# Optimization experiments

Hardware: AMD Instinct MI355X
Metric: run time of the kernel (lower is better)

Reference implementation:

```python
import jax, jax.numpy as jnp
import numpy as np

H = 8   # num_heads
K = 2   # num_timescales (hard-coded in module)


def _apply_rope(x, cos, sin):
    # x: [B,T,H,D]; cos/sin: [1,T,1,D/2]; interleaved even/odd pairs
    xp = x.reshape(*x.shape[:-1], -1, 2)
    xr, xi = xp[..., 0], xp[..., 1]
    rr = xr * cos - xi * sin
    ri = xr * sin + xi * cos
    return jnp.stack([rr, ri], axis=-1).reshape(x.shape)


def setup_inputs() -> dict:
    key = jax.random.key(0)
    ks = jax.random.split(key, 11)
    B, T, C = 4, 2048, 1024
    HK = H * K
    s = 0.02  # xavier-ish scale
    return {
        'x': jax.random.normal(ks[0], (B, T, C), jnp.float32),
        'mask': jnp.ones((B, T), jnp.int32),
        'Wq': jax.random.normal(ks[1], (C, C), jnp.float32) * s,
        'Wk': jax.random.normal(ks[2], (C, C), jnp.float32) * s,
        'Wv': jax.random.normal(ks[3], (C, C), jnp.float32) * s,
        'Wb': jax.random.normal(ks[4], (C, HK), jnp.float32) * s,
        'bb': jax.random.normal(ks[5], (HK,), jnp.float32) * 0.5 + 2.0,
        'Wm': jax.random.normal(ks[6], (C, HK), jnp.float32) * s,
        'bm': jax.random.normal(ks[7], (HK,), jnp.float32) * 0.1,
        'Wo': jax.random.normal(ks[8], (C, C), jnp.float32) * s,
        'bo': jnp.zeros((C,), jnp.float32),
    }


def reference(x, mask, Wq, Wk, Wv, Wb, bb, Wm, bm, Wo, bo):
    B, T, C = x.shape
    D = C // H
    q = (x @ Wq).reshape(B, T, H, D)
    k = (x @ Wk).reshape(B, T, H, D)
    v = (x @ Wv).reshape(B, T, H, D)

    # RoPE cache
    inv_freq = 1.0 / (10000.0 ** (jnp.arange(0, D, 2, dtype=jnp.float32) / D))
    freqs = jnp.arange(T, dtype=jnp.float32)[:, None] * inv_freq[None, :]  # [T,D/2]
    cos = jnp.cos(freqs)[None, :, None, :].astype(x.dtype)
    sin = jnp.sin(freqs)[None, :, None, :].astype(x.dtype)
    q = _apply_rope(q, cos, sin)
    k = _apply_rope(k, cos, sin)

    beta = jax.nn.sigmoid((x @ Wb + bb).reshape(B, T, H, K))  # [B,T,H,K]
    mix = jax.nn.softmax((x @ Wm + bm).reshape(B, T, H, K), axis=-1)

    def step(S, ins):
        # S: [B,H,K,D,D]
        q_t, k_t, v_t, b_t, m_t, mk = ins  # [B,H,D],[B,H,D],[B,H,D],[B,H,K],[B,H,K],[B]
        outer = jnp.einsum('bhd,bhe->bhde', k_t, v_t)          # [B,H,D,D]
        S_new = b_t[..., None, None] * S + outer[:, :, None]   # [B,H,K,D,D]
        S = jnp.where(mk[:, None, None, None, None] > 0, S_new, S)
        y_k = jnp.einsum('bhd,bhkde->bhke', q_t, S)            # [B,H,K,D]
        y_t = jnp.sum(y_k * m_t[..., None], axis=2)            # [B,H,D]
        y_t = jnp.where(mk[:, None, None] > 0, y_t, jnp.zeros_like(y_t))
        return S, y_t

    S0 = jnp.zeros((B, H, K, D, D), x.dtype)
    xs = (jnp.swapaxes(q, 0, 1), jnp.swapaxes(k, 0, 1), jnp.swapaxes(v, 0, 1),
          jnp.swapaxes(beta, 0, 1), jnp.swapaxes(mix, 0, 1), mask.T)
    _, ys = jax.lax.scan(step, S0, xs)           # ys: [T,B,H,D]
    y = jnp.swapaxes(ys, 0, 1).reshape(B, T, C)
    return y @ Wo + bo
```

## Files before the change

kernel.cpp:

```cpp
#include <hip/hip_runtime.h>

typedef __attribute__((ext_vector_type(4))) float f32x4;
typedef __attribute__((ext_vector_type(8))) __bf16 bf16x8;

#define T_DIM 2048
#define B_DIM 4
#define C_DIM 1024
#define H_N 8
#define D_H 128
#define M_ROWS 8192
#define MC ((size_t)M_ROWS * C_DIM)
#define LCH 64
#define NCH (T_DIM / LCH)
#define CHSZ (128 * 128)
#define SWE(r) ((((r) ^ ((r) >> 3)) & 7) << 3)

#define GLDS16(g, l) __builtin_amdgcn_global_load_lds( \
    (const __attribute__((address_space(1))) void*)(g), \
    (__attribute__((address_space(3))) void*)(l), 16, 0, 0)

__global__ void small_prep_k(float2* __restrict__ tab,
                             const float* __restrict__ Wb,
                             const float* __restrict__ Wm,
                             __bf16* __restrict__ WbmT) {
    int bid = blockIdx.x;
    if (bid < 512) {
        int idx = bid * 256 + threadIdx.x;
        int t = idx >> 6, i = idx & 63;
        float freq = expf(-(2.0f * (float)i / 128.0f) * 9.210340371976184f);
        float a = (float)t * freq;
        tab[idx] = make_float2(cosf(a), sinf(a));
    } else {
        int n = bid - 512;
        int col = n & 15;
        const float* W = (n < 16) ? Wb : Wm;
        for (int k = threadIdx.x; k < C_DIM; k += 256)
            WbmT[(size_t)n * C_DIM + k] = (__bf16)W[(size_t)k * 16 + col];
    }
}

__global__ __launch_bounds__(256) void cvt_x_k(const float* __restrict__ in,
                                               __bf16* __restrict__ out) {
    int i = blockIdx.x * 256 + threadIdx.x;
    f32x4 a = ((const f32x4*)in)[i * 2];
    f32x4 b = ((const f32x4*)in)[i * 2 + 1];
    bf16x8 o;
    o[0] = (__bf16)a.x; o[1] = (__bf16)a.y; o[2] = (__bf16)a.z; o[3] = (__bf16)a.w;
    o[4] = (__bf16)b.x; o[5] = (__bf16)b.y; o[6] = (__bf16)b.z; o[7] = (__bf16)b.w;
    ((bf16x8*)out)[i] = o;
}

__global__ __launch_bounds__(256) void wtrans_k(
    const float* __restrict__ W0, const float* __restrict__ W1,
    const float* __restrict__ W2, const float* __restrict__ W3,
    __bf16* __restrict__ out) {
    const float* W = blockIdx.z == 0 ? W0 : blockIdx.z == 1 ? W1 :
                     blockIdx.z == 2 ? W2 : W3;
    __bf16* o = out + (size_t)blockIdx.z * C_DIM * C_DIM;
    __shared__ float t[64][65];
    int tid = threadIdx.x;
    int r0 = blockIdx.y * 64, c0 = blockIdx.x * 64;
    #pragma unroll
    for (int it = 0; it < 4; ++it) {
        int idx = it * 256 + tid;
        int r = idx >> 4, c4 = (idx & 15) * 4;
        f32x4 v = *(const f32x4*)(W + (size_t)(r0 + r) * C_DIM + c0 + c4);
        t[r][c4] = v.x; t[r][c4 + 1] = v.y; t[r][c4 + 2] = v.z; t[r][c4 + 3] = v.w;
    }
    __syncthreads();
    #pragma unroll
    for (int it = 0; it < 2; ++it) {
        int idx = it * 256 + tid;
        int n = idx >> 3, k8 = (idx & 7) * 8;
        bf16x8 ov;
        #pragma unroll
        for (int j = 0; j < 8; ++j) ov[j] = (__bf16)t[k8 + j][n];
        *(bf16x8*)(o + (size_t)(c0 + n) * C_DIM + r0 + k8) = ov;
    }
}

__global__ __launch_bounds__(256) void betamix_mfma(
    const __bf16* __restrict__ xb, const __bf16* __restrict__ WbmT,
    const float* __restrict__ bb, const float* __restrict__ bm,
    float* __restrict__ beta, float* __restrict__ mix) {
    __shared__ __bf16 As[2][32 * 64];

    int tid = threadIdx.x;
    int w = tid >> 6, lane = tid & 63;
    int lr = lane & 15, lg = lane >> 4;
    int ifr = w >> 1, j = w & 1;
    int rows0 = blockIdx.x * 32;

    int srow = tid >> 3;
    int sg = (tid & 7) ^ (srow & 7);
    size_t aoff = (size_t)(rows0 + srow) * C_DIM + sg * 8;
    int ldso = w * 64 * 16;

    f32x4 acc = {};
    const __bf16* Wrow = WbmT + (size_t)(j * 16 + lr) * C_DIM;

    GLDS16(xb + aoff, (char*)As[0] + ldso);
    asm volatile("s_waitcnt vmcnt(0)" ::: "memory");
    __syncthreads();

    for (int t = 0; t < 16; ++t) {
        int cur = t & 1;
        if (t < 15) GLDS16(xb + aoff + (t + 1) * 64, (char*)As[cur ^ 1] + ldso);
        #pragma unroll
        for (int ss = 0; ss < 2; ++ss) {
            int ar = ifr * 16 + lr;
            bf16x8 af = *(const bf16x8*)((char*)As[cur] + ar * 128 + (((ss * 4 + lg) ^ (ar & 7)) << 4));
            bf16x8 bf = *(const bf16x8*)(Wrow + t * 64 + ss * 32 + lg * 8);
            acc = __builtin_amdgcn_mfma_f32_16x16x32_bf16(af, bf, acc, 0, 0, 0);
        }
        asm volatile("s_waitcnt vmcnt(0)" ::: "memory");
        __syncthreads();
    }

    float bias = (j ? bm : bb)[lr];
    #pragma unroll
    for (int r = 0; r < 4; ++r) {
        int row = rows0 + ifr * 16 + lg * 4 + r;
        float v = acc[r] + bias;
        if (j == 0) {
            beta[(size_t)row * 16 + lr] = 1.f / (1.f + expf(-v));
        } else {
            float other = __shfl_xor(v, 1);
            float mx = fmaxf(v, other);
            float e = expf(v - mx), eo = expf(other - mx);
            mix[(size_t)row * 16 + lr] = e / (e + eo);
        }
    }
}

__global__ __launch_bounds__(256) void decay_k(
    const float* __restrict__ beta, const float* __restrict__ mixp,
    const int* __restrict__ mask,
    float* __restrict__ wvm, float* __restrict__ rcm,
    float* __restrict__ qsc, float* __restrict__ cumLg) {
    int gw = blockIdx.x * 4 + (threadIdx.x >> 6);
    int s = threadIdx.x & 63;
    int scan = gw >> 5, c = gw & 31;
    int b = scan >> 4, hh = scan & 15;
    size_t row = (size_t)b * T_DIM + c * LCH + s;
    int mk = mask[row];
    float mf = mk ? 1.f : 0.f;
    float bt = mk ? beta[row * 16 + hh] : 1.f;
    float mx = mk ? mixp[row * 16 + hh] : 0.f;
    float cum = bt;
    #pragma unroll
    for (int off = 1; off < 64; off <<= 1) {
        float p = __shfl(cum, (s >= off) ? s - off : 0);
        if (s >= off) cum *= p;
    }
    float cl = __shfl(cum, 63);
    size_t o = (size_t)scan * T_DIM + c * LCH + s;
    wvm[o] = mf * cl / cum;
    rcm[o] = mf / cum;
    qsc[o] = mf * mx * cum;
    if (s == 63) cumLg[scan * NCH + c] = cl;
}

__global__ __launch_bounds__(256) void gemm_qkv(
    const __bf16* __restrict__ A, const __bf16* __restrict__ BT,
    __bf16* __restrict__ outq, const float2* __restrict__ rope_tab) {
    __shared__ __bf16 As[128 * 64];
    __shared__ __bf16 Bs[128 * 64];
    const int K = C_DIM;

    int tid = threadIdx.x;
    int xcd = blockIdx.x & 7, lid = blockIdx.x >> 3;
    int g = lid >> 6, u = lid & 63;
    int bm = xcd * 8 + (u >> 3), bn = g * 8 + (u & 7);
    int m_base = bm << 7, n_base = bn << 7;
    int w = tid >> 6, lane = tid & 63;
    int lr = lane & 15, lg = lane >> 4;
    int wm = (w >> 1) * 64, wn = (w & 1) * 64;

    size_t aoff[4], boff[4];
    int ldso[4];
    #pragma unroll
    for (int it = 0; it < 4; ++it) {
        int gi = it * 256 + tid;
        int row = gi >> 3;
        int gr = (gi & 7) ^ (row & 7);
        aoff[it] = (size_t)(m_base + row) * K + gr * 8;
        boff[it] = (size_t)(n_base + row) * K + gr * 8;
        ldso[it] = (it * 256 + w * 64) * 16;
    }

    f32x4 acc[4][4] = {};

    for (int k0 = 0; k0 < K; k0 += 64) {
        __syncthreads();
        #pragma unroll
        for (int it = 0; it < 4; ++it) {
            GLDS16(A + aoff[it] + k0, (char*)As + ldso[it]);
            GLDS16(BT + boff[it] + k0, (char*)Bs + ldso[it]);
        }
        __syncthreads();
        #pragma unroll
        for (int ss = 0; ss < 2; ++ss) {
            bf16x8 af[4], bfr[4];
            #pragma unroll
            for (int i = 0; i < 4; ++i) {
                int ar = wm + i * 16 + lr;
                af[i] = *(const bf16x8*)((char*)As + ar * 128 + (((ss * 4 + lg) ^ (ar & 7)) << 4));
                int br = wn + i * 16 + lr;
                bfr[i] = *(const bf16x8*)((char*)Bs + br * 128 + (((ss * 4 + lg) ^ (br & 7)) << 4));
            }
            #pragma unroll
            for (int i = 0; i < 4; ++i)
                #pragma unroll
                for (int j = 0; j < 4; ++j)
                    acc[i][j] = __builtin_amdgcn_mfma_f32_16x16x32_bf16(af[i], bfr[j], acc[i][j], 0, 0, 0);
        }
    }

    #pragma unroll
    for (int i = 0; i < 4; ++i) {
        #pragma unroll
        for (int j = 0; j < 4; ++j) {
            #pragma unroll
            for (int r = 0; r < 4; ++r) {
                int grow = m_base + wm + i * 16 + (lg << 2) + r;
                int gcol = n_base + wn + j * 16 + lr;
                float val = acc[i][j][r];
                int buf = gcol >> 10;
                int col = gcol & 1023;
                if (buf < 2) {
                    float partner = __shfl_xor(val, 1);
                    int t = grow & (T_DIM - 1);
                    int ii = (col & 127) >> 1;
                    float2 cs = rope_tab[t * 64 + ii];
                    val = (col & 1) ? (partner * cs.y + val * cs.x)
                                    : (val * cs.x - partner * cs.y);
                }
                outq[(size_t)buf * MC + (size_t)grow * C_DIM + col] = (__bf16)val;
            }
        }
    }
}

__global__ __launch_bounds__(256) void gemm_bt(
    const __bf16* __restrict__ A, const __bf16* __restrict__ BT,
    float* __restrict__ Cp, int M, int N, int K,
    const float* __restrict__ bias) {
    __shared__ __bf16 As[2][128 * 64];
    __shared__ __bf16 Bs[2][128 * 64];

    int tid = threadIdx.x;
    int nTN = N >> 7;
    int cpx = gridDim.x >> 3;
    int bid = ((int)blockIdx.x & 7) * cpx + ((int)blockIdx.x >> 3);
    int bm = bid / nTN, bn = bid % nTN;
    int m_base = bm << 7, n_base = bn << 7;
    int w = tid >> 6, lane = tid & 63;
    int lr = lane & 15, lg = lane >> 4;
    int wm = (w >> 1) * 64, wn = (w & 1) * 64;

    size_t aoff[4], boff[4];
    int ldso[4];
    #pragma unroll
    for (int it = 0; it < 4; ++it) {
        int gi = it * 256 + tid;
        int row = gi >> 3;
        int g = (gi & 7) ^ (row & 7);
        aoff[it] = (size_t)(m_base + row) * K + g * 8;
        boff[it] = (size_t)(n_base + row) * K + g * 8;
        ldso[it] = (it * 256 + w * 64) * 16;
    }

#define STAGE_G(bufi, k0)                                                   \
    _Pragma("unroll")                                                       \
    for (int it = 0; it < 4; ++it) {                                        \
        GLDS16(A + aoff[it] + (k0), (char*)As[bufi] + ldso[it]);            \
        GLDS16(BT + boff[it] + (k0), (char*)Bs[bufi] + ldso[it]);           \
    }

    f32x4 acc[4][4] = {};

    STAGE_G(0, 0);
    asm volatile("s_waitcnt vmcnt(0)" ::: "memory");
    __syncthreads();

    int nt = K >> 6;
    for (int t = 0; t < nt; ++t) {
        int cur = t & 1;
        if (t + 1 < nt) STAGE_G(cur ^ 1, (t + 1) * 64);
        #pragma unroll
        for (int ss = 0; ss < 2; ++ss) {
            bf16x8 af[4], bfr[4];
            #pragma unroll
            for (int i = 0; i < 4; ++i) {
                int ar = wm + i * 16 + lr;
                af[i] = *(const bf16x8*)((char*)As[cur] + ar * 128 + (((ss * 4 + lg) ^ (ar & 7)) << 4));
                int br = wn + i * 16 + lr;
                bfr[i] = *(const bf16x8*)((char*)Bs[cur] + br * 128 + (((ss * 4 + lg) ^ (br & 7)) << 4));
            }
            #pragma unroll
            for (int i = 0; i < 4; ++i)
                #pragma unroll
                for (int j = 0; j < 4; ++j)
                    acc[i][j] = __builtin_amdgcn_mfma_f32_16x16x32_bf16(af[i], bfr[j], acc[i][j], 0, 0, 0);
        }
        asm volatile("s_waitcnt vmcnt(0)" ::: "memory");
        __syncthreads();
    }
#undef STAGE_G

    #pragma unroll
    for (int i = 0; i < 4; ++i) {
        #pragma unroll
        for (int j = 0; j < 4; ++j) {
            #pragma unroll
            for (int r = 0; r < 4; ++r) {
                int grow = m_base + wm + i * 16 + (lg << 2) + r;
                int gcol = n_base + wn + j * 16 + lr;
                float val = acc[i][j][r] + bias[gcol];
                Cp[(size_t)grow * N + gcol] = val;
            }
        }
    }
}

__global__ __launch_bounds__(256) void chunk_sum_k(
    const __bf16* __restrict__ kg, const __bf16* __restrict__ vg,
    const float* __restrict__ wvm, __bf16* __restrict__ BT) {
    __shared__ __bf16 KT[128 * 64];
    __shared__ __bf16 VT[128 * 64];

    int tid = threadIdx.x;
    int c = blockIdx.x, kk = blockIdx.y, bh = blockIdx.z;
    int b = bh >> 3, h = bh & 7;
    int scan = bh * 2 + kk;
    size_t rowb = (size_t)b * T_DIM + c * LCH;
    size_t wb = (size_t)scan * T_DIM + c * LCH;

    #pragma unroll
    for (int it = 0; it < 4; ++it) {
        int f = tid + it * 256;
        int s = f >> 4, c8 = (f & 15) * 8;
        size_t g = (rowb + s) * C_DIM + h * D_H + c8;
        bf16x8 kv = *(const bf16x8*)(kg + g);
        bf16x8 vv = *(const bf16x8*)(vg + g);
        float ws_ = wvm[wb + s];
        #pragma unroll
        for (int j = 0; j < 8; ++j) {
            int d = c8 + j;
            KT[d * 64 + (s ^ SWE(d))] = (__bf16)(ws_ * (float)kv[j]);
            VT[d * 64 + (s ^ SWE(d))] = vv[j];
        }
    }
    __syncthreads();

    int w = tid >> 6, l = tid & 63;
    int lr = l & 15, lg = l >> 4;
    f32x4 acc[2][8] = {};
    #pragma unroll
    for (int kt = 0; kt < 2; ++kt) {
        int col = kt * 32 + lg * 8;
        bf16x8 aV[2], bK[8];
        #pragma unroll
        for (int et = 0; et < 2; ++et) {
            int e = w * 32 + et * 16 + lr;
            aV[et] = *(const bf16x8*)&VT[e * 64 + (col ^ SWE(e))];
        }
        #pragma unroll
        for (int dt = 0; dt < 8; ++dt) {
            int d = dt * 16 + lr;
            bK[dt] = *(const bf16x8*)&KT[d * 64 + (col ^ SWE(d))];
        }
        #pragma unroll
        for (int et = 0; et < 2; ++et)
            #pragma unroll
            for (int dt = 0; dt < 8; ++dt)
                acc[et][dt] = __builtin_amdgcn_mfma_f32_16x16x32_bf16(aV[et], bK[dt], acc[et][dt], 0, 0, 0);
    }

    __bf16* bout = BT + ((size_t)scan * NCH + c) * CHSZ;
    #pragma unroll
    for (int et = 0; et < 2; ++et)
        #pragma unroll
        for (int dt = 0; dt < 8; ++dt)
            #pragma unroll
            for (int r = 0; r < 4; ++r) {
                int e = w * 32 + et * 16 + lg * 4 + r;
                bout[e * 128 + dt * 16 + lr] = (__bf16)acc[et][dt][r];
            }
}

__global__ __launch_bounds__(256) void chunk_scan_k(
    __bf16* __restrict__ BT, const float* __restrict__ cumLg) {
    int bid = blockIdx.x;
    int scan = bid >> 3, part = bid & 7;
    int tid = threadIdx.x;
    int e = part * 16 + (tid >> 4);
    int d0 = (tid & 15) * 8;
    __bf16* base = BT + (size_t)scan * NCH * CHSZ + e * 128 + d0;
    const float* cl = cumLg + scan * NCH;
    float acc[8] = {};
    for (int c = 0; c < NCH; ++c) {
        bf16x8 bv = *(const bf16x8*)(base + (size_t)c * CHSZ);
        float g = cl[c];
        bf16x8 so;
        #pragma unroll
        for (int j = 0; j < 8; ++j) so[j] = (__bf16)acc[j];
        *(bf16x8*)(base + (size_t)c * CHSZ) = so;
        #pragma unroll
        for (int j = 0; j < 8; ++j) acc[j] = g * acc[j] + (float)bv[j];
    }
}

__global__ __launch_bounds__(256, 3) void chunk_out_k(
    const __bf16* __restrict__ qg, const __bf16* __restrict__ kg,
    const __bf16* __restrict__ vg, const __bf16* __restrict__ ST,
    const float* __restrict__ rcm, const float* __restrict__ qscg,
    __bf16* __restrict__ yg) {
    __shared__ __bf16 STs[2][64 * 128];
    __shared__ __bf16 VT[64 * 64];
    __shared__ __bf16 Ps[64 * 72];
    __shared__ float rcumf[2][64], qscf[2][64];

    int tid = threadIdx.x;
    int c = blockIdx.x, eh = blockIdx.y, bh = blockIdx.z;
    int b = bh >> 3, h = bh & 7;
    int e0 = eh * 64;
    size_t rowb = (size_t)b * T_DIM + c * LCH;
    int w = tid >> 6, l = tid & 63;
    int lr = l & 15, lg = l >> 4;

    {
        const __bf16* stb = ST + ((size_t)(bh * 2) * NCH + c) * CHSZ + (size_t)e0 * 128;
        int r = tid >> 4, gran = tid & 15;
        size_t goff = (size_t)r * 128 + ((gran ^ (r & 7)) * 8);
        #pragma unroll
        for (int kk = 0; kk < 2; ++kk) {
            const __bf16* sp = stb + (size_t)kk * NCH * CHSZ;
            #pragma unroll
            for (int it = 0; it < 4; ++it) {
                GLDS16(sp + goff + (size_t)it * 16 * 128,
                       (char*)STs[kk] + (it * 256 + w * 64) * 16);
            }
        }
    }

    if (tid < 128) {
        int s = tid & 63, kk = tid >> 6;
        size_t o = (size_t)(bh * 2 + kk) * T_DIM + c * LCH + s;
        rcumf[kk][s] = rcm[o];
        qscf[kk][s] = qscg[o];
    }

    bf16x8 vreg[2];
    #pragma unroll
    for (int it = 0; it < 2; ++it) {
        int f = tid + it * 256;
        int s = f >> 3, c8 = (f & 7) * 8;
        vreg[it] = *(const bf16x8*)(vg + (rowb + s) * C_DIM + h * D_H + e0 + c8);
    }

    const __bf16* qrow = qg + (rowb + w * 16 + lr) * C_DIM + h * D_H;
    bf16x8 aQ[4];
    #pragma unroll
    for (int kt = 0; kt < 4; ++kt)
        aQ[kt] = *(const bf16x8*)(qrow + kt * 32 + lg * 8);

    const __bf16* kbase = kg + rowb * C_DIM + h * D_H;
    bf16x8 bkreg[16];
    #pragma unroll
    for (int st = 0; st < 4; ++st)
        #pragma unroll
        for (int kt = 0; kt < 4; ++kt)
            bkreg[st * 4 + kt] = *(const bf16x8*)(kbase + (size_t)(st * 16 + lr) * C_DIM + kt * 32 + lg * 8);

    #pragma unroll
    for (int it = 0; it < 2; ++it) {
        int f = tid + it * 256;
        int s = f >> 3, c8 = (f & 7) * 8;
        #pragma unroll
        for (int j = 0; j < 8; ++j) {
            int el = c8 + j;
            VT[el * 64 + (s ^ SWE(el))] = vreg[it][j];
        }
    }

    f32x4 Praw[4];
    #pragma unroll
    for (int st = 0; st < 4; ++st) {
        f32x4 p = {};
        #pragma unroll
        for (int kt = 0; kt < 4; ++kt)
            p = __builtin_amdgcn_mfma_f32_16x16x32_bf16(aQ[kt], bkreg[st * 4 + kt], p, 0, 0, 0);
        Praw[st] = p;
    }

    asm volatile("s_waitcnt vmcnt(0)" ::: "memory");
    __syncthreads();

    f32x4 yA[4] = {};
    #pragma unroll
    for (int kk = 0; kk < 2; ++kk) {
        #pragma unroll
        for (int st = 0; st < 4; ++st) {
            #pragma unroll
            for (int r = 0; r < 4; ++r) {
                int tl = w * 16 + lg * 4 + r;
                int sc = st * 16 + lr;
                float pv = (sc <= tl) ? Praw[st][r] * rcumf[kk][sc] * qscf[kk][tl] : 0.f;
                Ps[tl * 72 + sc] = (__bf16)pv;
            }
        }
        bf16x8 aP[2];
        #pragma unroll
        for (int k2 = 0; k2 < 2; ++k2)
            aP[k2] = *(const bf16x8*)&Ps[(w * 16 + lr) * 72 + k2 * 32 + lg * 8];

        __builtin_amdgcn_s_setprio(1);
        #pragma unroll
        for (int et = 0; et < 4; ++et) {
            int el = et * 16 + lr;
            f32x4 ys = {};
            #pragma unroll
            for (int kt = 0; kt < 4; ++kt) {
                bf16x8 bs = *(const bf16x8*)((char*)STs[kk] + el * 256 + (((kt * 4 + lg) ^ (el & 7)) << 4));
                ys = __builtin_amdgcn_mfma_f32_16x16x32_bf16(aQ[kt], bs, ys, 0, 0, 0);
            }
            f32x4 yp = {};
            #pragma unroll
            for (int k2 = 0; k2 < 2; ++k2) {
                bf16x8 bv = *(const bf16x8*)&VT[el * 64 + ((k2 * 32 + lg * 8) ^ SWE(el))];
                yp = __builtin_amdgcn_mfma_f32_16x16x32_bf16(aP[k2], bv, yp, 0, 0, 0);
            }
            #pragma unroll
            for (int r = 0; r < 4; ++r)
                yA[et][r] += ys[r] * qscf[kk][w * 16 + lg * 4 + r] + yp[r];
        }
        __builtin_amdgcn_s_setprio(0);
    }
    #pragma unroll
    for (int et = 0; et < 4; ++et)
        #pragma unroll
        for (int r = 0; r < 4; ++r) {
            size_t row = rowb + w * 16 + lg * 4 + r;
            yg[row * C_DIM + h * D_H + e0 + et * 16 + lr] = (__bf16)yA[et][r];
        }
}

extern "C" void kernel_launch(void* const* d_in, const int* in_sizes, int n_in,
                              void* d_out, int out_size, void* d_ws, size_t ws_size,
                              hipStream_t stream) {
    const float* x    = (const float*)d_in[0];
    const int*   mask = (const int*)d_in[1];
    const float* Wq   = (const float*)d_in[2];
    const float* Wk   = (const float*)d_in[3];
    const float* Wv   = (const float*)d_in[4];
    const float* Wb   = (const float*)d_in[5];
    const float* bb   = (const float*)d_in[6];
    const float* Wm   = (const float*)d_in[7];
    const float* bm   = (const float*)d_in[8];
    const float* Wo   = (const float*)d_in[9];
    const float* bo   = (const float*)d_in[10];
    float* out = (float*)d_out;

    __bf16* q    = (__bf16*)d_ws;
    __bf16* k    = q + MC;
    __bf16* v    = k + MC;
    __bf16* xb   = v + MC;
    __bf16* WT   = xb + MC;
    __bf16* BT   = WT + (size_t)4 * C_DIM * C_DIM;
    float* beta  = (float*)(BT + (size_t)64 * NCH * CHSZ);
    float* mixb  = beta + M_ROWS * 16;
    float* cumL  = mixb + M_ROWS * 16;
    float* wvm   = cumL + 64 * NCH;
    float* rcm   = wvm + (size_t)64 * T_DIM;
    float* qscg  = rcm + (size_t)64 * T_DIM;
    float2* rope = (float2*)(qscg + (size_t)64 * T_DIM);
    __bf16* WbmT = (__bf16*)(rope + T_DIM * 64);
    __bf16* ysum = xb;

    small_prep_k<<<dim3(544), dim3(256), 0, stream>>>(rope, Wb, Wm, WbmT);
    cvt_x_k<<<dim3(MC / 8 / 256), dim3(256), 0, stream>>>(x, xb);
    wtrans_k<<<dim3(16, 16, 4), dim3(256), 0, stream>>>(Wq, Wk, Wv, Wo, WT);
    betamix_mfma<<<dim3(M_ROWS / 32), dim3(256), 0, stream>>>(xb, WbmT, bb, bm, beta, mixb);
    decay_k<<<dim3(512), dim3(256), 0, stream>>>(beta, mixb, mask, wvm, rcm, qscg, cumL);

    const size_t CC = (size_t)C_DIM * C_DIM;
    gemm_qkv<<<dim3(1536), dim3(256), 0, stream>>>(xb, WT, q, rope);

    chunk_sum_k<<<dim3(NCH, 2, 32), dim3(256), 0, stream>>>(k, v, wvm, BT);
    chunk_scan_k<<<dim3(512), dim3(256), 0, stream>>>(BT, cumL);
    chunk_out_k<<<dim3(NCH, 2, 32), dim3(256), 0, stream>>>(q, k, v, BT, rcm, qscg, ysum);

    gemm_bt<<<dim3((M_ROWS / 128) * (C_DIM / 128)), dim3(256), 0, stream>>>(
        ysum, WT + 3 * CC, out, M_ROWS, C_DIM, C_DIM, bo);
}
```

Measured before the change: 220.8 us.

## Merge prep kernels into one launch and double-buffer the QKV GEMM

The three small preprocessing kernels (x bf16 conversion, weight transposes, RoPE table and Wb/Wm transpose) become a single launch that branches on block index, removing two launch gaps. The QKV GEMM moves to a 3D grid with one z-slice per projection and double-buffered LDS staging, so the next K tile loads while MFMAs run on the current one. The block-to-tile mapping also changes to an XCD-interleaved scheme like gemm_bt. LDS use doubles to 64KB per block, which may lower occupancy, and the merged prep kernel allocates shared memory even for blocks that do not use it.

```diff
diff --git a/kernel.cpp b/kernel.cpp
--- a/kernel.cpp
+++ b/kernel.cpp
@@ -19,63 +19,63 @@
     (const __attribute__((address_space(1))) void*)(g), \
     (__attribute__((address_space(3))) void*)(l), 16, 0, 0)
 
-__global__ void small_prep_k(float2* __restrict__ tab,
-                             const float* __restrict__ Wb,
-                             const float* __restrict__ Wm,
-                             __bf16* __restrict__ WbmT) {
-    int bid = blockIdx.x;
-    if (bid < 512) {
-        int idx = bid * 256 + threadIdx.x;
-        int t = idx >> 6, i = idx & 63;
-        float freq = expf(-(2.0f * (float)i / 128.0f) * 9.210340371976184f);
-        float a = (float)t * freq;
-        tab[idx] = make_float2(cosf(a), sinf(a));
-    } else {
-        int n = bid - 512;
-        int col = n & 15;
-        const float* W = (n < 16) ? Wb : Wm;
-        for (int k = threadIdx.x; k < C_DIM; k += 256)
-            WbmT[(size_t)n * C_DIM + k] = (__bf16)W[(size_t)k * 16 + col];
-    }
-}
-
-__global__ __launch_bounds__(256) void cvt_x_k(const float* __restrict__ in,
-                                               __bf16* __restrict__ out) {
-    int i = blockIdx.x * 256 + threadIdx.x;
-    f32x4 a = ((const f32x4*)in)[i * 2];
-    f32x4 b = ((const f32x4*)in)[i * 2 + 1];
-    bf16x8 o;
-    o[0] = (__bf16)a.x; o[1] = (__bf16)a.y; o[2] = (__bf16)a.z; o[3] = (__bf16)a.w;
-    o[4] = (__bf16)b.x; o[5] = (__bf16)b.y; o[6] = (__bf16)b.z; o[7] = (__bf16)b.w;
-    ((bf16x8*)out)[i] = o;
-}
-
-__global__ __launch_bounds__(256) void wtrans_k(
+__global__ __launch_bounds__(256) void prep_all_k(
+    const float* __restrict__ x, __bf16* __restrict__ xb,
     const float* __restrict__ W0, const float* __restrict__ W1,
     const float* __restrict__ W2, const float* __restrict__ W3,
-    __bf16* __restrict__ out) {
-    const float* W = blockIdx.z == 0 ? W0 : blockIdx.z == 1 ? W1 :
-                     blockIdx.z == 2 ? W2 : W3;
-    __bf16* o = out + (size_t)blockIdx.z * C_DIM * C_DIM;
+    __bf16* __restrict__ WT,
+    float2* __restrict__ tab,
+    const float* __restrict__ Wb, const float* __restrict__ Wm,
+    __bf16* __restrict__ WbmT) {
     __shared__ float t[64][65];
+    int bid = blockIdx.x;
     int tid = threadIdx.x;
-    int r0 = blockIdx.y * 64, c0 = blockIdx.x * 64;
-    #pragma unroll
-    for (int it = 0; it < 4; ++it) {
-        int idx = it * 256 + tid;
-        int r = idx >> 4, c4 = (idx & 15) * 4;
-        f32x4 v = *(const f32x4*)(W + (size_t)(r0 + r) * C_DIM + c0 + c4);
-        t[r][c4] = v.x; t[r][c4 + 1] = v.y; t[r][c4 + 2] = v.z; t[r][c4 + 3] = v.w;
-    }
-    __syncthreads();
-    #pragma unroll
-    for (int it = 0; it < 2; ++it) {
-        int idx = it * 256 + tid;
-        int n = idx >> 3, k8 = (idx & 7) * 8;
-        bf16x8 ov;
-        #pragma unroll
-        for (int j = 0; j < 8; ++j) ov[j] = (__bf16)t[k8 + j][n];
-        *(bf16x8*)(o + (size_t)(c0 + n) * C_DIM + r0 + k8) = ov;
+    if (bid < 4096) {
+        int i = bid * 256 + tid;
+        f32x4 a = ((const f32x4*)x)[i * 2];
+        f32x4 b = ((const f32x4*)x)[i * 2 + 1];
+        bf16x8 o;
+        o[0] = (__bf16)a.x; o[1] = (__bf16)a.y; o[2] = (__bf16)a.z; o[3] = (__bf16)a.w;
+        o[4] = (__bf16)b.x; o[5] = (__bf16)b.y; o[6] = (__bf16)b.z; o[7] = (__bf16)b.w;
+        ((bf16x8*)xb)[i] = o;
+    } else if (bid < 5120) {
+        int tt = bid - 4096;
+        int wz = tt >> 8, rem = tt & 255;
+        int r0 = (rem >> 4) * 64, c0 = (rem & 15) * 64;
+        const float* W = wz == 0 ? W0 : wz == 1 ? W1 : wz == 2 ? W2 : W3;
+        __bf16* o = WT + (size_t)wz * C_DIM * C_DIM;
+        #pragma unroll
+        for (int it = 0; it < 4; ++it) {
+            int idx = it * 256 + tid;
+            int r = idx >> 4, c4 = (idx & 15) * 4;
+            f32x4 v = *(const f32x4*)(W + (size_t)(r0 + r) * C_DIM + c0 + c4);
+            t[r][c4] = v.x; t[r][c4 + 1] = v.y; t[r][c4 + 2] = v.z; t[r][c4 + 3] = v.w;
+        }
+        __syncthreads();
+        #pragma unroll
+        for (int it = 0; it < 2; ++it) {
+            int idx = it * 256 + tid;
+            int n = idx >> 3, k8 = (idx & 7) * 8;
+            bf16x8 ov;
+            #pragma unroll
+            for (int j = 0; j < 8; ++j) ov[j] = (__bf16)t[k8 + j][n];
+            *(bf16x8*)(o + (size_t)(c0 + n) * C_DIM + r0 + k8) = ov;
+        }
+    } else {
+        int sp = bid - 5120;
+        if (sp < 512) {
+            int idx = sp * 256 + tid;
+            int tq = idx >> 6, i = idx & 63;
+            float freq = expf(-(2.0f * (float)i / 128.0f) * 9.210340371976184f);
+            float a = (float)tq * freq;
+            tab[idx] = make_float2(cosf(a), sinf(a));
+        } else {
+            int n = sp - 512;
+            int col = n & 15;
+            const float* W = (n < 16) ? Wb : Wm;
+            for (int k = tid; k < C_DIM; k += 256)
+                WbmT[(size_t)n * C_DIM + k] = (__bf16)W[(size_t)k * 16 + col];
+        }
     }
 }
 
@@ -161,17 +161,22 @@
     if (s == 63) cumLg[scan * NCH + c] = cl;
 }
 
-__global__ __launch_bounds__(256) void gemm_qkv(
-    const __bf16* __restrict__ A, const __bf16* __restrict__ BT,
-    __bf16* __restrict__ outq, const float2* __restrict__ rope_tab) {
-    __shared__ __bf16 As[128 * 64];
-    __shared__ __bf16 Bs[128 * 64];
-    const int K = C_DIM;
+__global__ __launch_bounds__(256) void gemm_qkv3(
+    const __bf16* __restrict__ A, const __bf16* __restrict__ WT,
+    __bf16* __restrict__ outbase, const float2* __restrict__ rope_tab) {
+    __shared__ __bf16 As[2][128 * 64];
+    __shared__ __bf16 Bs[2][128 * 64];
+    const int K = C_DIM, N = C_DIM;
 
     int tid = threadIdx.x;
-    int xcd = blockIdx.x & 7, lid = blockIdx.x >> 3;
-    int g = lid >> 6, u = lid & 63;
-    int bm = xcd * 8 + (u >> 3), bn = g * 8 + (u & 7);
+    int z = blockIdx.z;
+    const __bf16* BT = WT + (size_t)z * C_DIM * C_DIM;
+    __bf16* Cp = outbase + (size_t)z * MC;
+    bool do_rope = z < 2;
+
+    int nTN = N >> 7;
+    int bid = ((int)blockIdx.x & 7) * 64 + ((int)blockIdx.x >> 3);
+    int bm = bid / nTN, bn = bid % nTN;
     int m_base = bm << 7, n_base = bn << 7;
     int w = tid >> 6, lane = tid & 63;
     int lr = lane & 15, lg = lane >> 4;
@@ -183,31 +188,38 @@
     for (int it = 0; it < 4; ++it) {
         int gi = it * 256 + tid;
         int row = gi >> 3;
-        int gr = (gi & 7) ^ (row & 7);
-        aoff[it] = (size_t)(m_base + row) * K + gr * 8;
-        boff[it] = (size_t)(n_base + row) * K + gr * 8;
+        int g = (gi & 7) ^ (row & 7);
+        aoff[it] = (size_t)(m_base + row) * K + g * 8;
+        boff[it] = (size_t)(n_base + row) * K + g * 8;
         ldso[it] = (it * 256 + w * 64) * 16;
     }
 
+#define STAGE_G(bufi, k0)                                                   \
+    _Pragma("unroll")                                                       \
+    for (int it = 0; it < 4; ++it) {                                        \
+        GLDS16(A + aoff[it] + (k0), (char*)As[bufi] + ldso[it]);            \
+        GLDS16(BT + boff[it] + (k0), (char*)Bs[bufi] + ldso[it]);           \
+    }
+
     f32x4 acc[4][4] = {};
 
-    for (int k0 = 0; k0 < K; k0 += 64) {
-        __syncthreads();
-        #pragma unroll
-        for (int it = 0; it < 4; ++it) {
-            GLDS16(A + aoff[it] + k0, (char*)As + ldso[it]);
-            GLDS16(BT + boff[it] + k0, (char*)Bs + ldso[it]);
-        }
-        __syncthreads();
+    STAGE_G(0, 0);
+    asm volatile("s_waitcnt vmcnt(0)" ::: "memory");
+    __syncthreads();
+
+    const int nt = K >> 6;
+    for (int t = 0; t < nt; ++t) {
+        int cur = t & 1;
+        if (t + 1 < nt) STAGE_G(cur ^ 1, (t + 1) * 64);
         #pragma unroll
         for (int ss = 0; ss < 2; ++ss) {
             bf16x8 af[4], bfr[4];
             #pragma unroll
             for (int i = 0; i < 4; ++i) {
                 int ar = wm + i * 16 + lr;
-                af[i] = *(const bf16x8*)((char*)As + ar * 128 + (((ss * 4 + lg) ^ (ar & 7)) << 4));
+                af[i] = *(const bf16x8*)((char*)As[cur] + ar * 128 + (((ss * 4 + lg) ^ (ar & 7)) << 4));
                 int br = wn + i * 16 + lr;
-                bfr[i] = *(const bf16x8*)((char*)Bs + br * 128 + (((ss * 4 + lg) ^ (br & 7)) << 4));
+                bfr[i] = *(const bf16x8*)((char*)Bs[cur] + br * 128 + (((ss * 4 + lg) ^ (br & 7)) << 4));
             }
             #pragma unroll
             for (int i = 0; i < 4; ++i)
@@ -215,7 +227,10 @@
                 for (int j = 0; j < 4; ++j)
                     acc[i][j] = __builtin_amdgcn_mfma_f32_16x16x32_bf16(af[i], bfr[j], acc[i][j], 0, 0, 0);
         }
-    }
+        asm volatile("s_waitcnt vmcnt(0)" ::: "memory");
+        __syncthreads();
+    }
+#undef STAGE_G
 
     #pragma unroll
     for (int i = 0; i < 4; ++i) {
@@ -226,17 +241,15 @@
                 int grow = m_base + wm + i * 16 + (lg << 2) + r;
                 int gcol = n_base + wn + j * 16 + lr;
                 float val = acc[i][j][r];
-                int buf = gcol >> 10;
-                int col = gcol & 1023;
-                if (buf < 2) {
+                if (do_rope) {
                     float partner = __shfl_xor(val, 1);
                     int t = grow & (T_DIM - 1);
-                    int ii = (col & 127) >> 1;
+                    int ii = (gcol & 127) >> 1;
                     float2 cs = rope_tab[t * 64 + ii];
-                    val = (col & 1) ? (partner * cs.y + val * cs.x)
-                                    : (val * cs.x - partner * cs.y);
+                    val = (gcol & 1) ? (partner * cs.y + val * cs.x)
+                                     : (val * cs.x - partner * cs.y);
                 }
-                outq[(size_t)buf * MC + (size_t)grow * C_DIM + col] = (__bf16)val;
+                Cp[(size_t)grow * C_DIM + gcol] = (__bf16)val;
             }
         }
     }
@@ -317,8 +330,7 @@
             for (int r = 0; r < 4; ++r) {
                 int grow = m_base + wm + i * 16 + (lg << 2) + r;
                 int gcol = n_base + wn + j * 16 + lr;
-                float val = acc[i][j][r] + bias[gcol];
-                Cp[(size_t)grow * N + gcol] = val;
+                Cp[(size_t)grow * N + gcol] = acc[i][j][r] + bias[gcol];
             }
         }
     }
@@ -579,14 +591,13 @@
     __bf16* WbmT = (__bf16*)(rope + T_DIM * 64);
     __bf16* ysum = xb;
 
-    small_prep_k<<<dim3(544), dim3(256), 0, stream>>>(rope, Wb, Wm, WbmT);
-    cvt_x_k<<<dim3(MC / 8 / 256), dim3(256), 0, stream>>>(x, xb);
-    wtrans_k<<<dim3(16, 16, 4), dim3(256), 0, stream>>>(Wq, Wk, Wv, Wo, WT);
+    prep_all_k<<<dim3(5664), dim3(256), 0, stream>>>(
+        x, xb, Wq, Wk, Wv, Wo, WT, rope, Wb, Wm, WbmT);
     betamix_mfma<<<dim3(M_ROWS / 32), dim3(256), 0, stream>>>(xb, WbmT, bb, bm, beta, mixb);
     decay_k<<<dim3(512), dim3(256), 0, stream>>>(beta, mixb, mask, wvm, rcm, qscg, cumL);
 
     const size_t CC = (size_t)C_DIM * C_DIM;
-    gemm_qkv<<<dim3(1536), dim3(256), 0, stream>>>(xb, WT, q, rope);
+    gemm_qkv3<<<dim3(512, 1, 3), dim3(256), 0, stream>>>(xb, WT, q, rope);
 
     chunk_sum_k<<<dim3(NCH, 2, 32), dim3(256), 0, stream>>>(k, v, wvm, BT);
     chunk_scan_k<<<dim3(512), dim3(256), 0, stream>>>(BT, cumL);
```

New measurement: 218.1 us. No clear change (-1.2%).

## Merge prep kernels into one launch and retile output GEMM to 64x128

Applied to the files above, without the earlier changes.

Three preprocessing kernels (x conversion, weight transposes, RoPE table and beta/mix weight packing) are folded into a single launch that dispatches on block index, cutting launch overhead and gaps between kernels. The output projection GEMM moves from 128x128 tiles with double-buffered LDS to 64x128 tiles with single buffering. This doubles the block count to 1024 for better CU occupancy and balance on an 8192x1024 output. In exchange, the GEMM loses global-load/compute overlap and re-reads B twice as often.

```diff
diff --git a/kernel.cpp b/kernel.cpp
--- a/kernel.cpp
+++ b/kernel.cpp
@@ -19,63 +19,63 @@
     (const __attribute__((address_space(1))) void*)(g), \
     (__attribute__((address_space(3))) void*)(l), 16, 0, 0)
 
-__global__ void small_prep_k(float2* __restrict__ tab,
-                             const float* __restrict__ Wb,
-                             const float* __restrict__ Wm,
-                             __bf16* __restrict__ WbmT) {
-    int bid = blockIdx.x;
-    if (bid < 512) {
-        int idx = bid * 256 + threadIdx.x;
-        int t = idx >> 6, i = idx & 63;
-        float freq = expf(-(2.0f * (float)i / 128.0f) * 9.210340371976184f);
-        float a = (float)t * freq;
-        tab[idx] = make_float2(cosf(a), sinf(a));
-    } else {
-        int n = bid - 512;
-        int col = n & 15;
-        const float* W = (n < 16) ? Wb : Wm;
-        for (int k = threadIdx.x; k < C_DIM; k += 256)
-            WbmT[(size_t)n * C_DIM + k] = (__bf16)W[(size_t)k * 16 + col];
-    }
-}
-
-__global__ __launch_bounds__(256) void cvt_x_k(const float* __restrict__ in,
-                                               __bf16* __restrict__ out) {
-    int i = blockIdx.x * 256 + threadIdx.x;
-    f32x4 a = ((const f32x4*)in)[i * 2];
-    f32x4 b = ((const f32x4*)in)[i * 2 + 1];
-    bf16x8 o;
-    o[0] = (__bf16)a.x; o[1] = (__bf16)a.y; o[2] = (__bf16)a.z; o[3] = (__bf16)a.w;
-    o[4] = (__bf16)b.x; o[5] = (__bf16)b.y; o[6] = (__bf16)b.z; o[7] = (__bf16)b.w;
-    ((bf16x8*)out)[i] = o;
-}
-
-__global__ __launch_bounds__(256) void wtrans_k(
+__global__ __launch_bounds__(256) void prep_all_k(
+    const float* __restrict__ x, __bf16* __restrict__ xb,
     const float* __restrict__ W0, const float* __restrict__ W1,
     const float* __restrict__ W2, const float* __restrict__ W3,
-    __bf16* __restrict__ out) {
-    const float* W = blockIdx.z == 0 ? W0 : blockIdx.z == 1 ? W1 :
-                     blockIdx.z == 2 ? W2 : W3;
-    __bf16* o = out + (size_t)blockIdx.z * C_DIM * C_DIM;
+    __bf16* __restrict__ WT,
+    float2* __restrict__ tab,
+    const float* __restrict__ Wb, const float* __restrict__ Wm,
+    __bf16* __restrict__ WbmT) {
     __shared__ float t[64][65];
-    int tid = threadIdx.x;
-    int r0 = blockIdx.y * 64, c0 = blockIdx.x * 64;
-    #pragma unroll
-    for (int it = 0; it < 4; ++it) {
-        int idx = it * 256 + tid;
-        int r = idx >> 4, c4 = (idx & 15) * 4;
-        f32x4 v = *(const f32x4*)(W + (size_t)(r0 + r) * C_DIM + c0 + c4);
-        t[r][c4] = v.x; t[r][c4 + 1] = v.y; t[r][c4 + 2] = v.z; t[r][c4 + 3] = v.w;
-    }
-    __syncthreads();
-    #pragma unroll
-    for (int it = 0; it < 2; ++it) {
-        int idx = it * 256 + tid;
-        int n = idx >> 3, k8 = (idx & 7) * 8;
-        bf16x8 ov;
-        #pragma unroll
-        for (int j = 0; j < 8; ++j) ov[j] = (__bf16)t[k8 + j][n];
-        *(bf16x8*)(o + (size_t)(c0 + n) * C_DIM + r0 + k8) = ov;
+    int bid = blockIdx.x;
+    int tid = threadIdx.x;
+    if (bid < 4096) {
+        int i = bid * 256 + tid;
+        f32x4 a = ((const f32x4*)x)[i * 2];
+        f32x4 b = ((const f32x4*)x)[i * 2 + 1];
+        bf16x8 o;
+        o[0] = (__bf16)a.x; o[1] = (__bf16)a.y; o[2] = (__bf16)a.z; o[3] = (__bf16)a.w;
+        o[4] = (__bf16)b.x; o[5] = (__bf16)b.y; o[6] = (__bf16)b.z; o[7] = (__bf16)b.w;
+        ((bf16x8*)xb)[i] = o;
+    } else if (bid < 5120) {
+        int tt = bid - 4096;
+        int wz = tt >> 8, rem = tt & 255;
+        int r0 = (rem >> 4) * 64, c0 = (rem & 15) * 64;
+        const float* W = wz == 0 ? W0 : wz == 1 ? W1 : wz == 2 ? W2 : W3;
+        __bf16* o = WT + (size_t)wz * C_DIM * C_DIM;
+        #pragma unroll
+        for (int it = 0; it < 4; ++it) {
+            int idx = it * 256 + tid;
+            int r = idx >> 4, c4 = (idx & 15) * 4;
+            f32x4 v = *(const f32x4*)(W + (size_t)(r0 + r) * C_DIM + c0 + c4);
+            t[r][c4] = v.x; t[r][c4 + 1] = v.y; t[r][c4 + 2] = v.z; t[r][c4 + 3] = v.w;
+        }
+        __syncthreads();
+        #pragma unroll
+        for (int it = 0; it < 2; ++it) {
+            int idx = it * 256 + tid;
+            int n = idx >> 3, k8 = (idx & 7) * 8;
+            bf16x8 ov;
+            #pragma unroll
+            for (int j = 0; j < 8; ++j) ov[j] = (__bf16)t[k8 + j][n];
+            *(bf16x8*)(o + (size_t)(c0 + n) * C_DIM + r0 + k8) = ov;
+        }
+    } else {
+        int sp = bid - 5120;
+        if (sp < 512) {
+            int idx = sp * 256 + tid;
+            int tq = idx >> 6, i = idx & 63;
+            float freq = expf(-(2.0f * (float)i / 128.0f) * 9.210340371976184f);
+            float a = (float)tq * freq;
+            tab[idx] = make_float2(cosf(a), sinf(a));
+        } else {
+            int n = sp - 512;
+            int col = n & 15;
+            const float* W = (n < 16) ? Wb : Wm;
+            for (int k = tid; k < C_DIM; k += 256)
+                WbmT[(size_t)n * C_DIM + k] = (__bf16)W[(size_t)k * 16 + col];
+        }
     }
 }
 
@@ -242,83 +242,81 @@
     }
 }
 
-__global__ __launch_bounds__(256) void gemm_bt(
+__global__ __launch_bounds__(256) void gemm_out64(
     const __bf16* __restrict__ A, const __bf16* __restrict__ BT,
-    float* __restrict__ Cp, int M, int N, int K,
-    const float* __restrict__ bias) {
-    __shared__ __bf16 As[2][128 * 64];
-    __shared__ __bf16 Bs[2][128 * 64];
-
-    int tid = threadIdx.x;
-    int nTN = N >> 7;
-    int cpx = gridDim.x >> 3;
-    int bid = ((int)blockIdx.x & 7) * cpx + ((int)blockIdx.x >> 3);
-    int bm = bid / nTN, bn = bid % nTN;
-    int m_base = bm << 7, n_base = bn << 7;
+    float* __restrict__ Cp, const float* __restrict__ bias) {
+    __shared__ __bf16 As[64 * 64];
+    __shared__ __bf16 Bs[128 * 64];
+    const int K = C_DIM, N = C_DIM;
+
+    int tid = threadIdx.x;
+    int bid = ((int)blockIdx.x & 7) * 128 + ((int)blockIdx.x >> 3);
+    int bm = bid >> 3, bn = bid & 7;
+    int m_base = bm << 6, n_base = bn << 7;
     int w = tid >> 6, lane = tid & 63;
     int lr = lane & 15, lg = lane >> 4;
-    int wm = (w >> 1) * 64, wn = (w & 1) * 64;
-
-    size_t aoff[4], boff[4];
-    int ldso[4];
+    int wm = (w >> 1) * 32, wn = (w & 1) * 64;
+
+    size_t aoff[2], boff[4];
+    int ldsoA[2], ldsoB[4];
+    #pragma unroll
+    for (int it = 0; it < 2; ++it) {
+        int gi = it * 256 + tid;
+        int row = gi >> 3;
+        int g = (gi & 7) ^ (row & 7);
+        aoff[it] = (size_t)(m_base + row) * K + g * 8;
+        ldsoA[it] = (it * 256 + w * 64) * 16;
+    }
     #pragma unroll
     for (int it = 0; it < 4; ++it) {
         int gi = it * 256 + tid;
         int row = gi >> 3;
         int g = (gi & 7) ^ (row & 7);
-        aoff[it] = (size_t)(m_base + row) * K + g * 8;
         boff[it] = (size_t)(n_base + row) * K + g * 8;
-        ldso[it] = (it * 256 + w * 64) * 16;
-    }
-
-#define STAGE_G(bufi, k0)                                                   \
-    _Pragma("unroll")                                                       \
-    for (int it = 0; it < 4; ++it) {                                        \
-        GLDS16(A + aoff[it] + (k0), (char*)As[bufi] + ldso[it]);            \
-        GLDS16(BT + boff[it] + (k0), (char*)Bs[bufi] + ldso[it]);           \
-    }
-
-    f32x4 acc[4][4] = {};
-
-    STAGE_G(0, 0);
-    asm volatile("s_waitcnt vmcnt(0)" ::: "memory");
-    __syncthreads();
-
-    int nt = K >> 6;
-    for (int t = 0; t < nt; ++t) {
-        int cur = t & 1;
-        if (t + 1 < nt) STAGE_G(cur ^ 1, (t + 1) * 64);
+        ldsoB[it] = (it * 256 + w * 64) * 16;
+    }
+
+    f32x4 acc[2][4] = {};
+
+    for (int k0 = 0; k0 < K; k0 += 64) {
+        __syncthreads();
+        #pragma unroll
+        for (int it = 0; it < 2; ++it)
+            GLDS16(A + aoff[it] + k0, (char*)As + ldsoA[it]);
+        #pragma unroll
+        for (int it = 0; it < 4; ++it)
+            GLDS16(BT + boff[it] + k0, (char*)Bs + ldsoB[it]);
+        __syncthreads();
         #pragma unroll
         for (int ss = 0; ss < 2; ++ss) {
-            bf16x8 af[4], bfr[4];
-            #pragma unroll
-            for (int i = 0; i < 4; ++i) {
+            bf16x8 af[2], bfr[4];
+            #pragma unroll
+            for (int i = 0; i < 2; ++i) {
                 int ar = wm + i * 16 + lr;
-                af[i] = *(const bf16x8*)((char*)As[cur] + ar * 128 + (((ss * 4 + lg) ^ (ar & 7)) << 4));
-                int br = wn + i * 16 + lr;
-                bfr[i] = *(const bf16x8*)((char*)Bs[cur] + br * 128 + (((ss * 4 + lg) ^ (br & 7)) << 4));
-            }
-            #pragma unroll
-            for (int i = 0; i < 4; ++i)
+                af[i] = *(const bf16x8*)((char*)As + ar * 128 + (((ss * 4 + lg) ^ (ar & 7)) << 4));
+            }
+            #pragma unroll
+            for (int j = 0; j < 4; ++j) {
+                int br = wn + j * 16 + lr;
+                bfr[j] = *(const bf16x8*)((char*)Bs + br * 128 + (((ss * 4 + lg) ^ (br & 7)) << 4));
+            }
+            #pragma unroll
+            for (int i = 0; i < 2; ++i)
                 #pragma unroll
                 for (int j = 0; j < 4; ++j)
                     acc[i][j] = __builtin_amdgcn_mfma_f32_16x16x32_bf16(af[i], bfr[j], acc[i][j], 0, 0, 0);
         }
-        asm volatile("s_waitcnt vmcnt(0)" ::: "memory");
-        __syncthreads();
-    }
-#undef STAGE_G
-
-    #pragma unroll
-    for (int i = 0; i < 4; ++i) {
+    }
+
+    #pragma unroll
+    for (int i = 0; i < 2; ++i) {
         #pragma unroll
         for (int j = 0; j < 4; ++j) {
             #pragma unroll
             for (int r = 0; r < 4; ++r) {
                 int grow = m_base + wm + i * 16 + (lg << 2) + r;
                 int gcol = n_base + wn + j * 16 + lr;
-                float val = acc[i][j][r] + bias[gcol];
-                Cp[(size_t)grow * N + gcol] = val;
+                Cp[(size_t)grow * N + gcol] = acc[i][j][r] + bias[gcol];
             }
         }
     }
@@ -579,9 +577,8 @@
     __bf16* WbmT = (__bf16*)(rope + T_DIM * 64);
     __bf16* ysum = xb;
 
-    small_prep_k<<<dim3(544), dim3(256), 0, stream>>>(rope, Wb, Wm, WbmT);
-    cvt_x_k<<<dim3(MC / 8 / 256), dim3(256), 0, stream>>>(x, xb);
-    wtrans_k<<<dim3(16, 16, 4), dim3(256), 0, stream>>>(Wq, Wk, Wv, Wo, WT);
+    prep_all_k<<<dim3(5664), dim3(256), 0, stream>>>(
+        x, xb, Wq, Wk, Wv, Wo, WT, rope, Wb, Wm, WbmT);
     betamix_mfma<<<dim3(M_ROWS / 32), dim3(256), 0, stream>>>(xb, WbmT, bb, bm, beta, mixb);
     decay_k<<<dim3(512), dim3(256), 0, stream>>>(beta, mixb, mask, wvm, rcm, qscg, cumL);
 
@@ -592,6 +589,5 @@
     chunk_scan_k<<<dim3(512), dim3(256), 0, stream>>>(BT, cumL);
     chunk_out_k<<<dim3(NCH, 2, 32), dim3(256), 0, stream>>>(q, k, v, BT, rcm, qscg, ysum);
 
-    gemm_bt<<<dim3((M_ROWS / 128) * (C_DIM / 128)), dim3(256), 0, stream>>>(
-        ysum, WT + 3 * CC, out, M_ROWS, C_DIM, C_DIM, bo);
-}
+    gemm_out64<<<dim3(1024), dim3(256), 0, stream>>>(ysum, WT + 3 * CC, out, bo);
+}
```

Measured after the change: 222.7 us. No clear change (+0.9%).
